# Kernel optimization log

Hardware: AMD Instinct MI355X
Metric: run time of the kernel (lower is better)

The kernel has to match this reference:

```python
import jax, jax.numpy as jnp
import numpy as np

N = 50000    # nodes
E = 800000   # edges
F = 128      # node_feature_dim
H = 128      # GCN hidden
H2 = 64      # fc1 hidden
T = 8        # num_tactics
G = 64       # graphs in batch


def setup_inputs() -> dict:
    key = jax.random.key(0)
    ks = jax.random.split(key, 12)
    s = 0.05
    return {
        "x": jax.random.normal(ks[0], (N, F), jnp.float32),
        "edge_index": jax.random.randint(ks[1], (2, E), 0, N, dtype=jnp.int32),
        "batch": jnp.sort(jax.random.randint(ks[2], (N,), 0, G, dtype=jnp.int32)),
        "W": jax.random.normal(ks[3], (F, H), jnp.float32) * s,
        "b": jax.random.normal(ks[4], (H,), jnp.float32) * s,
        "fc1_w": jax.random.normal(ks[5], (H, H2), jnp.float32) * s,
        "fc1_b": jax.random.normal(ks[6], (H2,), jnp.float32) * s,
        "actor_w": jax.random.normal(ks[7], (H2, T), jnp.float32) * s,
        "actor_b": jax.random.normal(ks[8], (T,), jnp.float32) * s,
        "critic_w": jax.random.normal(ks[9], (H2, 1), jnp.float32) * s,
        "critic_b": jax.random.normal(ks[10], (1,), jnp.float32) * s,
    }


def _gcn_conv(x, edge_index, W, b):
    # PyG GCNConv: add self-loops, symmetric D^-1/2 (A+I) D^-1/2 normalization,
    # linear transform first, then scatter-add aggregation, then bias.
    n = x.shape[0]
    loops = jnp.arange(n, dtype=edge_index.dtype)
    src = jnp.concatenate([edge_index[0], loops])  # message sources (x_j)
    dst = jnp.concatenate([edge_index[1], loops])  # aggregation targets
    deg = jax.ops.segment_sum(jnp.ones_like(dst, jnp.float32), dst, num_segments=N)
    dinv = deg ** -0.5  # deg >= 1 due to self-loops
    norm = dinv[src] * dinv[dst]                   # [E+N]
    h = x @ W                                      # [N, H]
    msgs = h[src] * norm[:, None]                  # [E+N, H]
    return jax.ops.segment_sum(msgs, dst, num_segments=N) + b


def reference(x, edge_index, batch, W, b, fc1_w, fc1_b, actor_w, actor_b, critic_w, critic_b):
    h = jax.nn.relu(_gcn_conv(x, edge_index, W, b))            # [N, H]
    # global_mean_pool over batch index
    sums = jax.ops.segment_sum(h, batch, num_segments=G)       # [G, H]
    cnts = jax.ops.segment_sum(jnp.ones((h.shape[0],), h.dtype), batch, num_segments=G)
    group_state = sums / jnp.maximum(cnts, 1.0)[:, None]
    z = jax.nn.relu(group_state @ fc1_w + fc1_b)               # [G, H2]
    tactic_probs = jax.nn.softmax(z @ actor_w + actor_b, axis=-1)  # [G, T]
    group_value = z @ critic_w + critic_b                      # [G, 1]
    return tactic_probs, group_value
```

## Files before the change

kernel.cpp:

```cpp
#include <hip/hip_runtime.h>
#include <hip/hip_bf16.h>

#define NN 50000
#define EE 800000
#define FF 128
#define HH 128
#define HID2 64
#define TT 8
#define GG 64
#define NB 196
#define NSB 256
#define EPB (EE / NSB)
#define NPAD 50048

using frag_ab = __attribute__((ext_vector_type(8))) short;
using frag_cd = __attribute__((ext_vector_type(4))) float;

__device__ inline unsigned short f2bf(float f) {
    union { float f; unsigned u; } v; v.f = f;
    unsigned r = v.u + 0x7fff + ((v.u >> 16) & 1);
    return (unsigned short)(r >> 16);
}

__global__ __launch_bounds__(256) void k_front(const int* __restrict__ dst,
                                               const float* __restrict__ W,
                                               int* __restrict__ table,
                                               unsigned short* __restrict__ wt_bf,
                                               float* __restrict__ gsum) {
    __shared__ int cnt[NB];
    int t = threadIdx.x, blk = blockIdx.x;
    if (blk < 64) {
        int gid = blk * 256 + t;
        int c = gid >> 7, k = gid & 127;
        wt_bf[gid] = f2bf(W[k * 128 + c]);
    }
    if (blk >= 64 && blk < 96) {
        int gid = (blk - 64) * 256 + t;
        gsum[gid] = 0.f;
    }
    for (int i = t; i < NB; i += 256) cnt[i] = 0;
    __syncthreads();
    int e0 = blk * EPB;
    for (int e = e0 + t; e < e0 + EPB; e += 256)
        atomicAdd(&cnt[dst[e] >> 8], 1);
    __syncthreads();
    for (int i = t; i < NB; i += 256) table[blk * NB + i] = cnt[i];
}

__global__ __launch_bounds__(256) void kb2a(int* __restrict__ table,
                                            int* __restrict__ ctot) {
    __shared__ int s[256];
    int t = threadIdx.x, b = blockIdx.x;
    int v = table[t * NB + b];
    s[t] = v;
    __syncthreads();
    for (int off = 1; off < 256; off <<= 1) {
        int a = s[t];
        int w = (t >= off) ? s[t - off] : 0;
        __syncthreads();
        s[t] = a + w;
        __syncthreads();
    }
    table[t * NB + b] = s[t] - v;
    if (t == 255) ctot[b] = s[255];
}

__global__ __launch_bounds__(256) void kb2b(const int* __restrict__ ctot,
                                            int* __restrict__ bbase) {
    __shared__ int s[256];
    int b = threadIdx.x;
    int v = (b < NB) ? ctot[b] : 0;
    s[b] = v;
    __syncthreads();
    for (int off = 1; off < 256; off <<= 1) {
        int a = s[b];
        int w = (b >= off) ? s[b - off] : 0;
        __syncthreads();
        s[b] = a + w;
        __syncthreads();
    }
    if (b < NB) bbase[b] = s[b] - v;
    if (b == 0) bbase[NB] = EE;
}

__global__ __launch_bounds__(256) void kb3(const int* __restrict__ src,
                                           const int* __restrict__ dst,
                                           const int* __restrict__ table,
                                           const int* __restrict__ bbase,
                                           unsigned* __restrict__ etmp) {
    __shared__ int ofs[NB];
    __shared__ int cur[NB];
    int t = threadIdx.x, blk = blockIdx.x;
    for (int i = t; i < NB; i += 256) {
        ofs[i] = table[blk * NB + i] + bbase[i];
        cur[i] = 0;
    }
    __syncthreads();
    int e0 = blk * EPB;
    for (int e = e0 + t; e < e0 + EPB; e += 256) {
        int d = dst[e];
        int b = d >> 8;
        int r = atomicAdd(&cur[b], 1);
        etmp[ofs[b] + r] = ((unsigned)d << 16) | (unsigned)src[e];
    }
}

__global__ __launch_bounds__(256) void k_csr(const unsigned* __restrict__ etmp,
                                             const int* __restrict__ bbase,
                                             int* __restrict__ row_ptr,
                                             float* __restrict__ dinv,
                                             int* __restrict__ srcs) {
    __shared__ int s[256];
    __shared__ int cur[256];
    int t = threadIdx.x, b = blockIdx.x;
    s[t] = 0;
    __syncthreads();
    int e0 = bbase[b], e1 = bbase[b + 1];
    for (int e = e0 + t; e < e1; e += 256)
        atomicAdd(&s[(etmp[e] >> 16) & 255], 1);
    __syncthreads();
    int v = s[t];
    for (int off = 1; off < 256; off <<= 1) {
        int a = s[t];
        int w = (t >= off) ? s[t - off] : 0;
        __syncthreads();
        s[t] = a + w;
        __syncthreads();
    }
    int excl = s[t] - v + e0;
    int node = b * 256 + t;
    if (node < NN) {
        row_ptr[node] = excl;
        dinv[node] = rsqrtf((float)(v + 1));
    }
    if (b == NB - 1 && t == 0) row_ptr[NN] = EE;
    cur[t] = excl;
    __syncthreads();
    for (int e = e0 + t; e < e1; e += 256) {
        unsigned u = etmp[e];
        int slot = atomicAdd(&cur[(u >> 16) & 255], 1);
        srcs[slot] = (int)(u & 0xffffu);
    }
}

__global__ __launch_bounds__(256) void k_gemm(const float* __restrict__ x,
                                              const unsigned short* __restrict__ wt_bf,
                                              const float* __restrict__ dinv,
                                              unsigned short* __restrict__ hs) {
    int tid = threadIdx.x;
    int w = tid >> 6, lane = tid & 63;
    int m = lane & 15, quad = lane >> 4;
    int r0 = blockIdx.x * 64 + w * 16;
    int row = r0 + m;
    frag_cd acc[8];
#pragma unroll
    for (int nt = 0; nt < 8; nt++) acc[nt] = frag_cd{0.f, 0.f, 0.f, 0.f};

#pragma unroll
    for (int k0 = 0; k0 < 128; k0 += 32) {
        unsigned short av[8];
        if (row < NN) {
            const float4* p = (const float4*)(x + (size_t)row * 128 + k0 + quad * 8);
            float4 a0 = p[0], a1 = p[1];
            av[0] = f2bf(a0.x); av[1] = f2bf(a0.y); av[2] = f2bf(a0.z); av[3] = f2bf(a0.w);
            av[4] = f2bf(a1.x); av[5] = f2bf(a1.y); av[6] = f2bf(a1.z); av[7] = f2bf(a1.w);
        } else {
#pragma unroll
            for (int j = 0; j < 8; j++) av[j] = 0;
        }
        frag_ab a = *(const frag_ab*)av;
#pragma unroll
        for (int nt = 0; nt < 8; nt++) {
            frag_ab bfr = *(const frag_ab*)(wt_bf + (size_t)(nt * 16 + m) * 128 + k0 + quad * 8);
            acc[nt] = __builtin_amdgcn_mfma_f32_16x16x32_bf16(a, bfr, acc[nt], 0, 0, 0);
        }
    }
#pragma unroll
    for (int reg = 0; reg < 4; reg++) {
        int gr = r0 + quad * 4 + reg;
        if (gr < NN) {
            float di = dinv[gr];
#pragma unroll
            for (int nt = 0; nt < 8; nt++)
                hs[(size_t)gr * 128 + nt * 16 + m] = f2bf(acc[nt][reg] * di);
        }
    }
}

#define ACC8(u) \
    a0 += __uint_as_float((u).x << 16); a1 += __uint_as_float((u).x & 0xffff0000u); \
    a2 += __uint_as_float((u).y << 16); a3 += __uint_as_float((u).y & 0xffff0000u); \
    a4 += __uint_as_float((u).z << 16); a5 += __uint_as_float((u).z & 0xffff0000u); \
    a6 += __uint_as_float((u).w << 16); a7 += __uint_as_float((u).w & 0xffff0000u);

__global__ __launch_bounds__(256) void k_aggr(const uint4* __restrict__ hs4,
                                              const int* __restrict__ row_ptr,
                                              const int* __restrict__ srcs,
                                              const float* __restrict__ dinv,
                                              const float* __restrict__ bias,
                                              const int* __restrict__ batch,
                                              float* __restrict__ gsum) {
    __shared__ float gacc[8 * 128];
    int tid = threadIdx.x;
    int qid = tid >> 4, sub = tid & 15;
    int i_base = blockIdx.x * 16;
    int g_first = batch[i_base];
    int last = i_base + 15; if (last >= NN) last = NN - 1;
    int gspan = batch[last] - g_first + 1;
    bool lds_pool = (gspan <= 8);
    int slots = lds_pool ? gspan : 0;
    for (int idx = tid; idx < slots * 128; idx += 256) gacc[idx] = 0.f;
    __syncthreads();

    const float4* b4 = (const float4*)(bias + sub * 8);
    float4 bb0 = b4[0], bb1 = b4[1];

    int i = i_base + qid;
    if (i < NN) {
        int lg = batch[i] - g_first;
        float di = dinv[i];
        uint4 su = hs4[(size_t)i * 16 + sub];
        float a0 = __uint_as_float(su.x << 16);
        float a1 = __uint_as_float(su.x & 0xffff0000u);
        float a2 = __uint_as_float(su.y << 16);
        float a3 = __uint_as_float(su.y & 0xffff0000u);
        float a4 = __uint_as_float(su.z << 16);
        float a5 = __uint_as_float(su.z & 0xffff0000u);
        float a6 = __uint_as_float(su.w << 16);
        float a7 = __uint_as_float(su.w & 0xffff0000u);
        int e = row_ptr[i], e1 = row_ptr[i + 1];
        for (; e + 7 < e1; e += 8) {
            int s0 = srcs[e],     s1 = srcs[e + 1], s2 = srcs[e + 2], s3 = srcs[e + 3];
            int s4 = srcs[e + 4], s5 = srcs[e + 5], s6 = srcs[e + 6], s7 = srcs[e + 7];
            uint4 u0 = hs4[(size_t)s0 * 16 + sub];
            uint4 u1 = hs4[(size_t)s1 * 16 + sub];
            uint4 u2 = hs4[(size_t)s2 * 16 + sub];
            uint4 u3 = hs4[(size_t)s3 * 16 + sub];
            uint4 u4 = hs4[(size_t)s4 * 16 + sub];
            uint4 u5 = hs4[(size_t)s5 * 16 + sub];
            uint4 u6 = hs4[(size_t)s6 * 16 + sub];
            uint4 u7 = hs4[(size_t)s7 * 16 + sub];
            ACC8(u0) ACC8(u1) ACC8(u2) ACC8(u3)
            ACC8(u4) ACC8(u5) ACC8(u6) ACC8(u7)
        }
        for (; e + 3 < e1; e += 4) {
            int s0 = srcs[e], s1 = srcs[e + 1], s2 = srcs[e + 2], s3 = srcs[e + 3];
            uint4 u0 = hs4[(size_t)s0 * 16 + sub];
            uint4 u1 = hs4[(size_t)s1 * 16 + sub];
            uint4 u2 = hs4[(size_t)s2 * 16 + sub];
            uint4 u3 = hs4[(size_t)s3 * 16 + sub];
            ACC8(u0) ACC8(u1) ACC8(u2) ACC8(u3)
        }
        for (; e < e1; ++e) {
            uint4 u0 = hs4[(size_t)srcs[e] * 16 + sub];
            ACC8(u0)
        }
        float r0 = fmaxf(fmaf(a0, di, bb0.x), 0.f);
        float r1 = fmaxf(fmaf(a1, di, bb0.y), 0.f);
        float r2 = fmaxf(fmaf(a2, di, bb0.z), 0.f);
        float r3 = fmaxf(fmaf(a3, di, bb0.w), 0.f);
        float r4 = fmaxf(fmaf(a4, di, bb1.x), 0.f);
        float r5 = fmaxf(fmaf(a5, di, bb1.y), 0.f);
        float r6 = fmaxf(fmaf(a6, di, bb1.z), 0.f);
        float r7 = fmaxf(fmaf(a7, di, bb1.w), 0.f);
        float* gp = lds_pool ? &gacc[lg * 128 + sub * 8]
                             : &gsum[(g_first + lg) * 128 + sub * 8];
        atomicAdd(&gp[0], r0);
        atomicAdd(&gp[1], r1);
        atomicAdd(&gp[2], r2);
        atomicAdd(&gp[3], r3);
        atomicAdd(&gp[4], r4);
        atomicAdd(&gp[5], r5);
        atomicAdd(&gp[6], r6);
        atomicAdd(&gp[7], r7);
    }
    __syncthreads();
    for (int idx = tid; idx < slots * 128; idx += 256) {
        float v = gacc[idx];
        if (v != 0.f)
            atomicAdd(&gsum[(g_first + (idx >> 7)) * 128 + (idx & 127)], v);
    }
}

__device__ inline int lbound(const int* __restrict__ a, int n, int key) {
    int lo = 0, hi = n;
    while (lo < hi) {
        int mid = (lo + hi) >> 1;
        if (a[mid] < key) lo = mid + 1;
        else hi = mid;
    }
    return lo;
}

__global__ __launch_bounds__(64) void k_head(const float* __restrict__ gsum,
                                             const int* __restrict__ batch,
                                             const float* __restrict__ fc1_w,
                                             const float* __restrict__ fc1_b,
                                             const float* __restrict__ actor_w,
                                             const float* __restrict__ actor_b,
                                             const float* __restrict__ critic_w,
                                             const float* __restrict__ critic_b,
                                             float* __restrict__ out) {
    __shared__ float gs[128];
    __shared__ float zs[64];
    __shared__ float ls[8], es[8];
    int g = blockIdx.x, t = threadIdx.x;
    int lo = lbound(batch, NN, g), hi = lbound(batch, NN, g + 1);
    float invc = 1.f / fmaxf((float)(hi - lo), 1.f);
    gs[t] = gsum[g * 128 + t] * invc;
    gs[t + 64] = gsum[g * 128 + 64 + t] * invc;
    __syncthreads();
    float z = fc1_b[t];
    for (int k = 0; k < 128; k++) z = fmaf(gs[k], fc1_w[k * 64 + t], z);
    zs[t] = fmaxf(z, 0.f);
    __syncthreads();
    if (t < 8) {
        float l = actor_b[t];
        for (int k = 0; k < 64; k++) l = fmaf(zs[k], actor_w[k * 8 + t], l);
        ls[t] = l;
    }
    __syncthreads();
    if (t < 8) {
        float m = ls[0];
#pragma unroll
        for (int j = 1; j < 8; j++) m = fmaxf(m, ls[j]);
        es[t] = expf(ls[t] - m);
    }
    __syncthreads();
    if (t < 8) {
        float ssum = 0.f;
#pragma unroll
        for (int j = 0; j < 8; j++) ssum += es[j];
        out[g * 8 + t] = es[t] / ssum;
    }
    if (t == 32) {
        float v = critic_b[0];
        for (int k = 0; k < 64; k++) v = fmaf(zs[k], critic_w[k], v);
        out[GG * TT + g] = v;
    }
}

extern "C" void kernel_launch(void* const* d_in, const int* in_sizes, int n_in,
                              void* d_out, int out_size, void* d_ws, size_t ws_size,
                              hipStream_t stream) {
    const float* x        = (const float*)d_in[0];
    const int*   ei       = (const int*)d_in[1];
    const int*   batch    = (const int*)d_in[2];
    const float* W        = (const float*)d_in[3];
    const float* b        = (const float*)d_in[4];
    const float* fc1_w    = (const float*)d_in[5];
    const float* fc1_b    = (const float*)d_in[6];
    const float* actor_w  = (const float*)d_in[7];
    const float* actor_b  = (const float*)d_in[8];
    const float* critic_w = (const float*)d_in[9];
    const float* critic_b = (const float*)d_in[10];
    float* out = (float*)d_out;

    char* ws = (char*)d_ws;
    size_t off = 0;
    unsigned short* hs    = (unsigned short*)(ws + off); off += (size_t)NN * 128 * 2 + 64;
    unsigned short* wt_bf = (unsigned short*)(ws + off); off += (size_t)128 * 128 * 2;
    float* dinv      = (float*)(ws + off);    off += (size_t)NN * 4;
    int*   row_ptr   = (int*)(ws + off);      off += (size_t)(NN + 1) * 4 + 12;
    int*   srcs      = (int*)(ws + off);      off += (size_t)EE * 4;
    unsigned* etmp   = (unsigned*)(ws + off); off += (size_t)EE * 4;
    int*   table     = (int*)(ws + off);      off += (size_t)NSB * NB * 4;
    int*   bbase     = (int*)(ws + off);      off += (size_t)(NB + 1) * 4 + 12;
    int*   ctot      = (int*)(ws + off);      off += (size_t)NB * 4 + 16;
    float* gsum      = (float*)(ws + off);    off += (size_t)GG * HH * 4;

    const int* src = ei;
    const int* dst = ei + EE;

    k_front<<<NSB, 256, 0, stream>>>(dst, W, table, wt_bf, gsum);
    kb2a<<<NB, 256, 0, stream>>>(table, ctot);
    kb2b<<<1, 256, 0, stream>>>(ctot, bbase);
    kb3<<<NSB, 256, 0, stream>>>(src, dst, table, bbase, etmp);
    k_csr<<<NB, 256, 0, stream>>>(etmp, bbase, row_ptr, dinv, srcs);
    k_gemm<<<NPAD / 64, 256, 0, stream>>>(x, wt_bf, dinv, hs);
    k_aggr<<<(NN + 15) / 16, 256, 0, stream>>>((const uint4*)hs, row_ptr, srcs,
                                               dinv, b, batch, gsum);
    k_head<<<GG, 64, 0, stream>>>(gsum, batch, fc1_w, fc1_b, actor_w, actor_b,
                                  critic_w, critic_b, out);
}
```

Before: 201.0 us.

## Assign one wavefront per node in aggregation, splitting edges across four lane groups

The aggregation kernel now gives each node a full 64-lane wavefront instead of a 16-lane group. The four quarter-groups each gather a different edge of the neighbour list, and the partial sums are combined with cross-lane shuffles. This raises memory-level parallelism per node and evens out imbalance between high- and low-degree nodes, which targets the latency-bound gather. The cost is idle lanes for nodes with few edges, shuffle overhead, and a clamped tail load that may fetch redundant rows. It also relies on NN dividing evenly by 8.

```diff
diff --git a/kernel.cpp b/kernel.cpp
--- a/kernel.cpp
+++ b/kernel.cpp
@@ -193,7 +193,7 @@
     a4 += __uint_as_float((u).z << 16); a5 += __uint_as_float((u).z & 0xffff0000u); \
     a6 += __uint_as_float((u).w << 16); a7 += __uint_as_float((u).w & 0xffff0000u);
 
-__global__ __launch_bounds__(256) void k_aggr(const uint4* __restrict__ hs4,
+__global__ __launch_bounds__(512) void k_aggr(const uint4* __restrict__ hs4,
                                               const int* __restrict__ row_ptr,
                                               const int* __restrict__ srcs,
                                               const float* __restrict__ dinv,
@@ -202,67 +202,84 @@
                                               float* __restrict__ gsum) {
     __shared__ float gacc[8 * 128];
     int tid = threadIdx.x;
-    int qid = tid >> 4, sub = tid & 15;
-    int i_base = blockIdx.x * 16;
+    int wid = tid >> 6;
+    int lane = tid & 63;
+    int q = lane >> 4, sub = lane & 15;
+    int i_base = blockIdx.x * 8;
+    int i = i_base + wid;
     int g_first = batch[i_base];
-    int last = i_base + 15; if (last >= NN) last = NN - 1;
-    int gspan = batch[last] - g_first + 1;
+    int gspan = batch[i_base + 7] - g_first + 1;
     bool lds_pool = (gspan <= 8);
     int slots = lds_pool ? gspan : 0;
-    for (int idx = tid; idx < slots * 128; idx += 256) gacc[idx] = 0.f;
-    __syncthreads();
-
+    for (int idx = tid; idx < slots * 128; idx += 512) gacc[idx] = 0.f;
+    __syncthreads();
+
+    int lg = batch[i] - g_first;
+    float di = dinv[i];
+    uint4 su = hs4[(size_t)i * 16 + sub];
+    int e = row_ptr[i], e1 = row_ptr[i + 1];
     const float4* b4 = (const float4*)(bias + sub * 8);
     float4 bb0 = b4[0], bb1 = b4[1];
 
-    int i = i_base + qid;
-    if (i < NN) {
-        int lg = batch[i] - g_first;
-        float di = dinv[i];
-        uint4 su = hs4[(size_t)i * 16 + sub];
-        float a0 = __uint_as_float(su.x << 16);
-        float a1 = __uint_as_float(su.x & 0xffff0000u);
-        float a2 = __uint_as_float(su.y << 16);
-        float a3 = __uint_as_float(su.y & 0xffff0000u);
-        float a4 = __uint_as_float(su.z << 16);
-        float a5 = __uint_as_float(su.z & 0xffff0000u);
-        float a6 = __uint_as_float(su.w << 16);
-        float a7 = __uint_as_float(su.w & 0xffff0000u);
-        int e = row_ptr[i], e1 = row_ptr[i + 1];
-        for (; e + 7 < e1; e += 8) {
-            int s0 = srcs[e],     s1 = srcs[e + 1], s2 = srcs[e + 2], s3 = srcs[e + 3];
-            int s4 = srcs[e + 4], s5 = srcs[e + 5], s6 = srcs[e + 6], s7 = srcs[e + 7];
-            uint4 u0 = hs4[(size_t)s0 * 16 + sub];
-            uint4 u1 = hs4[(size_t)s1 * 16 + sub];
-            uint4 u2 = hs4[(size_t)s2 * 16 + sub];
-            uint4 u3 = hs4[(size_t)s3 * 16 + sub];
-            uint4 u4 = hs4[(size_t)s4 * 16 + sub];
-            uint4 u5 = hs4[(size_t)s5 * 16 + sub];
-            uint4 u6 = hs4[(size_t)s6 * 16 + sub];
-            uint4 u7 = hs4[(size_t)s7 * 16 + sub];
-            ACC8(u0) ACC8(u1) ACC8(u2) ACC8(u3)
-            ACC8(u4) ACC8(u5) ACC8(u6) ACC8(u7)
-        }
-        for (; e + 3 < e1; e += 4) {
-            int s0 = srcs[e], s1 = srcs[e + 1], s2 = srcs[e + 2], s3 = srcs[e + 3];
-            uint4 u0 = hs4[(size_t)s0 * 16 + sub];
-            uint4 u1 = hs4[(size_t)s1 * 16 + sub];
-            uint4 u2 = hs4[(size_t)s2 * 16 + sub];
-            uint4 u3 = hs4[(size_t)s3 * 16 + sub];
-            ACC8(u0) ACC8(u1) ACC8(u2) ACC8(u3)
-        }
-        for (; e < e1; ++e) {
-            uint4 u0 = hs4[(size_t)srcs[e] * 16 + sub];
-            ACC8(u0)
-        }
-        float r0 = fmaxf(fmaf(a0, di, bb0.x), 0.f);
-        float r1 = fmaxf(fmaf(a1, di, bb0.y), 0.f);
-        float r2 = fmaxf(fmaf(a2, di, bb0.z), 0.f);
-        float r3 = fmaxf(fmaf(a3, di, bb0.w), 0.f);
-        float r4 = fmaxf(fmaf(a4, di, bb1.x), 0.f);
-        float r5 = fmaxf(fmaf(a5, di, bb1.y), 0.f);
-        float r6 = fmaxf(fmaf(a6, di, bb1.z), 0.f);
-        float r7 = fmaxf(fmaf(a7, di, bb1.w), 0.f);
+    float a0 = 0.f, a1 = 0.f, a2 = 0.f, a3 = 0.f,
+          a4 = 0.f, a5 = 0.f, a6 = 0.f, a7 = 0.f;
+
+    for (; e + 16 <= e1; e += 16) {
+        int s0 = srcs[e + q];
+        int s1 = srcs[e + 4 + q];
+        int s2 = srcs[e + 8 + q];
+        int s3 = srcs[e + 12 + q];
+        uint4 u0 = hs4[(size_t)s0 * 16 + sub];
+        uint4 u1 = hs4[(size_t)s1 * 16 + sub];
+        uint4 u2 = hs4[(size_t)s2 * 16 + sub];
+        uint4 u3 = hs4[(size_t)s3 * 16 + sub];
+        ACC8(u0) ACC8(u1) ACC8(u2) ACC8(u3)
+    }
+    if (e < e1) {
+        int last = e1 - 1;
+        int i0 = e + q;      int c0 = (i0 <= last) ? i0 : last;
+        int i1 = e + 4 + q;  int c1 = (i1 <= last) ? i1 : last;
+        int i2 = e + 8 + q;  int c2 = (i2 <= last) ? i2 : last;
+        int i3 = e + 12 + q; int c3 = (i3 <= last) ? i3 : last;
+        int s0 = srcs[c0], s1 = srcs[c1], s2 = srcs[c2], s3 = srcs[c3];
+        uint4 u0 = hs4[(size_t)s0 * 16 + sub];
+        uint4 u1 = hs4[(size_t)s1 * 16 + sub];
+        uint4 u2 = hs4[(size_t)s2 * 16 + sub];
+        uint4 u3 = hs4[(size_t)s3 * 16 + sub];
+        if (i0 <= last) { ACC8(u0) }
+        if (i1 <= last) { ACC8(u1) }
+        if (i2 <= last) { ACC8(u2) }
+        if (i3 <= last) { ACC8(u3) }
+    }
+
+    a0 += __shfl_xor(a0, 16); a0 += __shfl_xor(a0, 32);
+    a1 += __shfl_xor(a1, 16); a1 += __shfl_xor(a1, 32);
+    a2 += __shfl_xor(a2, 16); a2 += __shfl_xor(a2, 32);
+    a3 += __shfl_xor(a3, 16); a3 += __shfl_xor(a3, 32);
+    a4 += __shfl_xor(a4, 16); a4 += __shfl_xor(a4, 32);
+    a5 += __shfl_xor(a5, 16); a5 += __shfl_xor(a5, 32);
+    a6 += __shfl_xor(a6, 16); a6 += __shfl_xor(a6, 32);
+    a7 += __shfl_xor(a7, 16); a7 += __shfl_xor(a7, 32);
+
+    a0 += __uint_as_float(su.x << 16);
+    a1 += __uint_as_float(su.x & 0xffff0000u);
+    a2 += __uint_as_float(su.y << 16);
+    a3 += __uint_as_float(su.y & 0xffff0000u);
+    a4 += __uint_as_float(su.z << 16);
+    a5 += __uint_as_float(su.z & 0xffff0000u);
+    a6 += __uint_as_float(su.w << 16);
+    a7 += __uint_as_float(su.w & 0xffff0000u);
+
+    float r0 = fmaxf(fmaf(a0, di, bb0.x), 0.f);
+    float r1 = fmaxf(fmaf(a1, di, bb0.y), 0.f);
+    float r2 = fmaxf(fmaf(a2, di, bb0.z), 0.f);
+    float r3 = fmaxf(fmaf(a3, di, bb0.w), 0.f);
+    float r4 = fmaxf(fmaf(a4, di, bb1.x), 0.f);
+    float r5 = fmaxf(fmaf(a5, di, bb1.y), 0.f);
+    float r6 = fmaxf(fmaf(a6, di, bb1.z), 0.f);
+    float r7 = fmaxf(fmaf(a7, di, bb1.w), 0.f);
+
+    if (q == 0) {
         float* gp = lds_pool ? &gacc[lg * 128 + sub * 8]
                              : &gsum[(g_first + lg) * 128 + sub * 8];
         atomicAdd(&gp[0], r0);
@@ -275,7 +292,7 @@
         atomicAdd(&gp[7], r7);
     }
     __syncthreads();
-    for (int idx = tid; idx < slots * 128; idx += 256) {
+    for (int idx = tid; idx < slots * 128; idx += 512) {
         float v = gacc[idx];
         if (v != 0.f)
             atomicAdd(&gsum[(g_first + (idx >> 7)) * 128 + (idx & 127)], v);
@@ -378,8 +395,8 @@
     kb3<<<NSB, 256, 0, stream>>>(src, dst, table, bbase, etmp);
     k_csr<<<NB, 256, 0, stream>>>(etmp, bbase, row_ptr, dinv, srcs);
     k_gemm<<<NPAD / 64, 256, 0, stream>>>(x, wt_bf, dinv, hs);
-    k_aggr<<<(NN + 15) / 16, 256, 0, stream>>>((const uint4*)hs, row_ptr, srcs,
-                                               dinv, b, batch, gsum);
+    k_aggr<<<NN / 8, 512, 0, stream>>>((const uint4*)hs, row_ptr, srcs,
+                                       dinv, b, batch, gsum);
     k_head<<<GG, 64, 0, stream>>>(gsum, batch, fc1_w, fc1_b, actor_w, actor_b,
                                   critic_w, critic_b, out);
 }
```

Result: no change. 204.8 us (+1.9%).
